# Kernel optimization log

Measured on AMD Instinct MI355X. Metric: run time of the kernel, lower is better.

Reference implementation:

```python
import jax, jax.numpy as jnp
import numpy as np

N = 8192
D_IN = 512
D_OUT = 64
ALPHA = 0.2  # LeakyReLU negative slope
MASK_VAL = -9e15


def setup_inputs() -> dict:
    key = jax.random.key(0)
    k1, k2, k3, k4 = jax.random.split(key, 4)
    inp = jax.random.normal(k1, (N, D_IN), dtype=jnp.float32)
    adj = (jax.random.uniform(k2, (N, N)) < 0.05).astype(jnp.float32)
    adj = adj.at[jnp.arange(N), jnp.arange(N)].set(1.0)
    W = jax.random.normal(k3, (D_IN, D_OUT), dtype=jnp.float32) * 0.05
    a = jax.random.normal(k4, (2 * D_OUT, 1), dtype=jnp.float32) * 0.05
    return {"input": inp, "adj": adj, "W": W, "a": a}


def reference(input, adj, W, a):
    # h = input @ W : [n, out]
    h = input @ W
    # Algebraic equivalent of the dense pairwise concat:
    # e_ij = leakyrelu([h_i || h_j] . a) = leakyrelu(h_i.a1 + h_j.a2)
    a1, a2 = a[:D_OUT, 0], a[D_OUT:, 0]          # [out], [out]
    e = jax.nn.leaky_relu(
        (h @ a1)[:, None] + (h @ a2)[None, :],    # [n, n]
        negative_slope=ALPHA,
    )
    attention = jnp.where(adj > 0, e, MASK_VAL)
    attention = jax.nn.softmax(attention, axis=1)
    out = attention @ h                            # [n, out]
    return jax.nn.elu(out)                         # end=False branch
```

## Files before the change

### kernel.cpp

```cpp
#include <hip/hip_runtime.h>
#include <hip/hip_bf16.h>

#define N 8192
#define D_IN 512
#define D_OUT 64
#define ALPHA 0.2f
#define BM 16
#define NSPLIT 4
#define KSEG (N / NSPLIT)
#define NSH (KSEG / 128)

typedef __attribute__((ext_vector_type(4))) float f32x4;
typedef __attribute__((ext_vector_type(8))) short bf16x8;

static __device__ __forceinline__ unsigned pk_bf16(float lo, float hi) {
    unsigned ulo = __bfloat16_as_ushort(__float2bfloat16(lo));
    unsigned uhi = __bfloat16_as_ushort(__float2bfloat16(hi));
    return (uhi << 16) | ulo;
}

__global__ __launch_bounds__(256) void gat_prep_kernel(
    const float* __restrict__ input, const float* __restrict__ adj,
    const float* __restrict__ W, const float* __restrict__ a,
    unsigned short* __restrict__ hpk, float* __restrict__ s1,
    float* __restrict__ s2, unsigned char* __restrict__ msk)
{
    if (blockIdx.x < 512) {
        int wave = (blockIdx.x * 256 + threadIdx.x) >> 6;
        int lane = threadIdx.x & 63;
        int row0 = wave * 4;
        const float* in0 = input + (size_t)row0 * D_IN;
        float a1 = a[lane], a2 = a[D_OUT + lane];
        float acc[4];
#pragma unroll
        for (int r = 0; r < 4; ++r) acc[r] = 0.f;
#pragma unroll 4
        for (int k = 0; k < D_IN; ++k) {
            float wk = W[k * D_OUT + lane];
#pragma unroll
            for (int r = 0; r < 4; ++r)
                acc[r] = fmaf(in0[(size_t)r * D_IN + k], wk, acc[r]);
        }
        {
            int kw = row0 >> 5, kb = (row0 >> 3) & 3, e0 = row0 & 7;
            int dw = lane >> 4, dd = lane & 15;
            size_t off = ((size_t)((kw * 4 + dw) * 64) + kb * 16 + dd) * 8 + e0;
            uint2 hv;
            hv.x = pk_bf16(acc[0], acc[1]);
            hv.y = pk_bf16(acc[2], acc[3]);
            *(uint2*)(hpk + off) = hv;
        }
#pragma unroll
        for (int r = 0; r < 4; ++r) {
            float p1 = acc[r] * a1;
            float p2 = acc[r] * a2;
#pragma unroll
            for (int off = 32; off; off >>= 1) {
                p1 += __shfl_xor(p1, off, 64);
                p2 += __shfl_xor(p2, off, 64);
            }
            if (lane == 0) { s1[row0 + r] = p1; s2[row0 + r] = p2; }
        }
    } else {
        size_t wave = (((size_t)blockIdx.x - 512) * 256 + threadIdx.x) >> 6;
        int lane = threadIdx.x & 63;
#pragma unroll 4
        for (int it = 0; it < 16; ++it) {
            size_t fo = (wave * 16 + it) * 512 + (size_t)lane * 8;
            float4 v0 = *(const float4*)(adj + fo);
            float4 v1 = *(const float4*)(adj + fo + 4);
            unsigned b =  (unsigned)(v0.x > 0.f)
                       | ((unsigned)(v0.y > 0.f) << 1)
                       | ((unsigned)(v0.z > 0.f) << 2)
                       | ((unsigned)(v0.w > 0.f) << 3)
                       | ((unsigned)(v1.x > 0.f) << 4)
                       | ((unsigned)(v1.y > 0.f) << 5)
                       | ((unsigned)(v1.z > 0.f) << 6)
                       | ((unsigned)(v1.w > 0.f) << 7);
            msk[fo >> 3] = (unsigned char)b;
        }
    }
}

struct MSP { unsigned m; float4 sA, sB; };
struct UBP { uint4 b0, b1, b2, b3; };

static __device__ __forceinline__ void issue_ms(MSP& p, const unsigned char* mb,
                                                const float* sb, int ps) {
    p.m  = mb[ps * 16];
    p.sA = *(const float4*)(sb + ps * 128);
    p.sB = *(const float4*)(sb + ps * 128 + 4);
}
static __device__ __forceinline__ void issue_ub(UBP& p, const unsigned short* hb,
                                                int ps) {
    const unsigned short* f = hb + ((size_t)ps << 13);
    p.b0 = *(const uint4*)(f);
    p.b1 = *(const uint4*)(f + 512);
    p.b2 = *(const uint4*)(f + 1024);
    p.b3 = *(const uint4*)(f + 1536);
}

__global__ __launch_bounds__(256, 4) void gat_flash_kernel(
    const unsigned char* __restrict__ msk, const unsigned short* __restrict__ hpk,
    const float* __restrict__ s1, const float* __restrict__ s2,
    float* __restrict__ pacc, float* __restrict__ plsum)
{
    __shared__ float Cl[4][BM][D_OUT];
    __shared__ float lsl[4][BM];

    const int tid  = threadIdx.x;
    const int lane = tid & 63;
    const int ws   = tid >> 6;
    const int i    = lane & 15;
    const int kb   = lane >> 4;
    const int hf   = blockIdx.x >> 9;
    const int rb   = blockIdx.x & 511;
    const int rg   = rb * BM + i;

    const int col0 = hf * KSEG + ws * 32 + kb * 8;
    const unsigned char* mb_lane = msk + ((size_t)rg << 10) + (col0 >> 3);
    const float* s2_lane = s2 + col0;
    const unsigned short* hb_lane =
        hpk + (((size_t)(hf * 64 + ws)) << 11) + (lane << 3);

    float s1r  = s1[rg];
    float eref = s1r + s2[rg];
    eref = eref > 0.f ? eref : ALPHA * eref;
    float lsum = 0.f;
    f32x4 acc0 = {0,0,0,0}, acc1 = {0,0,0,0}, acc2 = {0,0,0,0}, acc3 = {0,0,0,0};

    auto step = [&](const MSP& p, const UBP& u) {
        const float* sv0 = (const float*)&p.sA;
        const float* sv1 = (const float*)&p.sB;
        float w[8];
#pragma unroll
        for (int z = 0; z < 4; ++z) {
            float e0 = s1r + sv0[z]; e0 = e0 > 0.f ? e0 : ALPHA * e0;
            float e1 = s1r + sv1[z]; e1 = e1 > 0.f ? e1 : ALPHA * e1;
            float w0 = __expf(e0 - eref);
            float w1 = __expf(e1 - eref);
            w[z]     = ((p.m >> z) & 1u)       ? w0 : 0.f;
            w[z + 4] = ((p.m >> (z + 4)) & 1u) ? w1 : 0.f;
        }
#pragma unroll
        for (int z = 0; z < 8; ++z) lsum += w[z];
        uint4 pk;
        pk.x = pk_bf16(w[0], w[1]); pk.y = pk_bf16(w[2], w[3]);
        pk.z = pk_bf16(w[4], w[5]); pk.w = pk_bf16(w[6], w[7]);
        bf16x8 A = __builtin_bit_cast(bf16x8, pk);
        acc0 = __builtin_amdgcn_mfma_f32_16x16x32_bf16(A, __builtin_bit_cast(bf16x8, u.b0), acc0, 0, 0, 0);
        acc1 = __builtin_amdgcn_mfma_f32_16x16x32_bf16(A, __builtin_bit_cast(bf16x8, u.b1), acc1, 0, 0, 0);
        acc2 = __builtin_amdgcn_mfma_f32_16x16x32_bf16(A, __builtin_bit_cast(bf16x8, u.b2), acc2, 0, 0, 0);
        acc3 = __builtin_amdgcn_mfma_f32_16x16x32_bf16(A, __builtin_bit_cast(bf16x8, u.b3), acc3, 0, 0, 0);
    };

    MSP M0, M1; UBP U0, U1;
    issue_ms(M0, mb_lane, s2_lane, 0); issue_ub(U0, hb_lane, 0);
    issue_ms(M1, mb_lane, s2_lane, 1); issue_ub(U1, hb_lane, 1);
#pragma unroll 2
    for (int p = 0; p < NSH; p += 2) {
        step(M0, U0);
        if (p + 2 < NSH) { issue_ms(M0, mb_lane, s2_lane, p + 2); issue_ub(U0, hb_lane, p + 2); }
        step(M1, U1);
        if (p + 3 < NSH) { issue_ms(M1, mb_lane, s2_lane, p + 3); issue_ub(U1, hb_lane, p + 3); }
    }

    lsum += __shfl_xor(lsum, 16, 64);
    lsum += __shfl_xor(lsum, 32, 64);
    if (lane < 16) lsl[ws][lane] = lsum;

    const f32x4 av[4] = {acc0, acc1, acc2, acc3};
#pragma unroll
    for (int dw = 0; dw < 4; ++dw)
#pragma unroll
        for (int reg = 0; reg < 4; ++reg)
            Cl[ws][kb * 4 + reg][dw * 16 + i] = av[dw][reg];
    __syncthreads();

#pragma unroll
    for (int o = tid; o < BM * D_OUT; o += 256) {
        int row = o >> 6, d = o & 63;
        float v = (Cl[0][row][d] + Cl[1][row][d]) + (Cl[2][row][d] + Cl[3][row][d]);
        pacc[((size_t)hf * N + rb * BM + row) * 64 + d] = v;
    }
    if (tid < BM)
        plsum[hf * N + rb * BM + tid] =
            (lsl[0][tid] + lsl[1][tid]) + (lsl[2][tid] + lsl[3][tid]);
}

__global__ __launch_bounds__(256) void gat_reduce_kernel(
    const float* __restrict__ pacc, const float* __restrict__ plsum,
    float* __restrict__ out)
{
    int idx = blockIdx.x * 256 + threadIdx.x;
    int row = idx >> 6;
    float aa = 0.f, l = 0.f;
#pragma unroll
    for (int hf = 0; hf < NSPLIT; ++hf) {
        aa += pacc[(size_t)hf * N * 64 + idx];
        l  += plsum[hf * N + row];
    }
    float o = aa / l;
    out[idx] = o > 0.f ? o : expm1f(o);
}

extern "C" void kernel_launch(void* const* d_in, const int* in_sizes, int n_in,
                              void* d_out, int out_size, void* d_ws, size_t ws_size,
                              hipStream_t stream) {
    const float* input = (const float*)d_in[0];
    const float* adj   = (const float*)d_in[1];
    const float* W     = (const float*)d_in[2];
    const float* a     = (const float*)d_in[3];
    float* out = (float*)d_out;

    unsigned short* hpk = (unsigned short*)d_ws;
    float* s1    = (float*)(hpk + (size_t)N * D_OUT);
    float* s2    = s1 + N;
    float* pacc  = s2 + N;
    float* plsum = pacc + (size_t)NSPLIT * N * 64;
    unsigned char* msk = (unsigned char*)(plsum + NSPLIT * N);

    gat_prep_kernel<<<2560, 256, 0, stream>>>(input, adj, W, a, hpk, s1, s2, msk);
    gat_flash_kernel<<<512 * NSPLIT, 256, 0, stream>>>(msk, hpk, s1, s2, pacc, plsum);
    gat_reduce_kernel<<<N * 64 / 256, 256, 0, stream>>>(pacc, plsum, out);
}
```

Before: 124.1 us.

## Split prep into mask and h kernels, enlarge flash row tile, drop LDS reduction

```diff
diff --git a/kernel.cpp b/kernel.cpp
--- a/kernel.cpp
+++ b/kernel.cpp
@@ -5,10 +5,11 @@
 #define D_IN 512
 #define D_OUT 64
 #define ALPHA 0.2f
-#define BM 16
+#define BM 64
 #define NSPLIT 4
 #define KSEG (N / NSPLIT)
 #define NSH (KSEG / 128)
+#define NSLICE (NSPLIT * 4)
 
 typedef __attribute__((ext_vector_type(4))) float f32x4;
 typedef __attribute__((ext_vector_type(8))) short bf16x8;
@@ -19,75 +20,88 @@
     return (uhi << 16) | ulo;
 }
 
-__global__ __launch_bounds__(256) void gat_prep_kernel(
-    const float* __restrict__ input, const float* __restrict__ adj,
-    const float* __restrict__ W, const float* __restrict__ a,
-    unsigned short* __restrict__ hpk, float* __restrict__ s1,
-    float* __restrict__ s2, unsigned char* __restrict__ msk)
-{
-    if (blockIdx.x < 512) {
-        int wave = (blockIdx.x * 256 + threadIdx.x) >> 6;
-        int lane = threadIdx.x & 63;
-        int row0 = wave * 4;
-        const float* in0 = input + (size_t)row0 * D_IN;
+__global__ __launch_bounds__(256) void gat_mask_kernel(
+    const float* __restrict__ adj, unsigned char* __restrict__ msk)
+{
+    size_t wave = ((size_t)blockIdx.x * 256 + threadIdx.x) >> 6;
+    int lane = threadIdx.x & 63;
+#pragma unroll
+    for (int it = 0; it < 8; ++it) {
+        size_t fo = (wave * 8 + it) * 512 + (size_t)lane * 8;
+        float4 v0 = *(const float4*)(adj + fo);
+        float4 v1 = *(const float4*)(adj + fo + 4);
+        unsigned b =  (unsigned)(v0.x > 0.f)
+                   | ((unsigned)(v0.y > 0.f) << 1)
+                   | ((unsigned)(v0.z > 0.f) << 2)
+                   | ((unsigned)(v0.w > 0.f) << 3)
+                   | ((unsigned)(v1.x > 0.f) << 4)
+                   | ((unsigned)(v1.y > 0.f) << 5)
+                   | ((unsigned)(v1.z > 0.f) << 6)
+                   | ((unsigned)(v1.w > 0.f) << 7);
+        msk[fo >> 3] = (unsigned char)b;
+    }
+}
+
+__global__ __launch_bounds__(256) void gat_h_kernel(
+    const float* __restrict__ input, const float* __restrict__ W,
+    const float* __restrict__ a, unsigned short* __restrict__ hpk,
+    float* __restrict__ s1, float* __restrict__ s2)
+{
+    __shared__ float hp[4][4][64];
+    int ws   = threadIdx.x >> 6;
+    int lane = threadIdx.x & 63;
+    int row0 = blockIdx.x * 4;
+    const float* in0 = input + (size_t)row0 * D_IN + ws * 128;
+    const float* Wp  = W + ws * 128 * D_OUT;
+    float acc[4] = {0.f, 0.f, 0.f, 0.f};
+#pragma unroll 4
+    for (int k = 0; k < 128; ++k) {
+        float wk = Wp[k * D_OUT + lane];
+#pragma unroll
+        for (int r = 0; r < 4; ++r)
+            acc[r] = fmaf(in0[r * D_IN + k], wk, acc[r]);
+    }
+#pragma unroll
+    for (int r = 0; r < 4; ++r) hp[ws][r][lane] = acc[r];
+    __syncthreads();
+    if (ws == 0) {
+        float h[4];
+#pragma unroll
+        for (int r = 0; r < 4; ++r)
+            h[r] = (hp[0][r][lane] + hp[1][r][lane]) + (hp[2][r][lane] + hp[3][r][lane]);
+        int kw = row0 >> 5, kb = (row0 >> 3) & 3, e0 = row0 & 7;
+        int dw = lane >> 4, dd = lane & 15;
+        size_t off = ((size_t)((kw * 4 + dw) * 64) + kb * 16 + dd) * 8 + e0;
+        uint2 hv;
+        hv.x = pk_bf16(h[0], h[1]);
+        hv.y = pk_bf16(h[2], h[3]);
+        *(uint2*)(hpk + off) = hv;
         float a1 = a[lane], a2 = a[D_OUT + lane];
-        float acc[4];
-#pragma unroll
-        for (int r = 0; r < 4; ++r) acc[r] = 0.f;
-#pragma unroll 4
-        for (int k = 0; k < D_IN; ++k) {
-            float wk = W[k * D_OUT + lane];
-#pragma unroll
-            for (int r = 0; r < 4; ++r)
-                acc[r] = fmaf(in0[(size_t)r * D_IN + k], wk, acc[r]);
-        }
-        {
-            int kw = row0 >> 5, kb = (row0 >> 3) & 3, e0 = row0 & 7;
-            int dw = lane >> 4, dd = lane & 15;
-            size_t off = ((size_t)((kw * 4 + dw) * 64) + kb * 16 + dd) * 8 + e0;
-            uint2 hv;
-            hv.x = pk_bf16(acc[0], acc[1]);
-            hv.y = pk_bf16(acc[2], acc[3]);
-            *(uint2*)(hpk + off) = hv;
-        }
 #pragma unroll
         for (int r = 0; r < 4; ++r) {
-            float p1 = acc[r] * a1;
-            float p2 = acc[r] * a2;
-#pragma unroll
-            for (int off = 32; off; off >>= 1) {
-                p1 += __shfl_xor(p1, off, 64);
-                p2 += __shfl_xor(p2, off, 64);
+            float p1 = h[r] * a1;
+            float p2 = h[r] * a2;
+#pragma unroll
+            for (int off2 = 32; off2; off2 >>= 1) {
+                p1 += __shfl_xor(p1, off2, 64);
+                p2 += __shfl_xor(p2, off2, 64);
             }
             if (lane == 0) { s1[row0 + r] = p1; s2[row0 + r] = p2; }
         }
-    } else {
-        size_t wave = (((size_t)blockIdx.x - 512) * 256 + threadIdx.x) >> 6;
-        int lane = threadIdx.x & 63;
-#pragma unroll 4
-        for (int it = 0; it < 16; ++it) {
-            size_t fo = (wave * 16 + it) * 512 + (size_t)lane * 8;
-            float4 v0 = *(const float4*)(adj + fo);
-            float4 v1 = *(const float4*)(adj + fo + 4);
-            unsigned b =  (unsigned)(v0.x > 0.f)
-                       | ((unsigned)(v0.y > 0.f) << 1)
-                       | ((unsigned)(v0.z > 0.f) << 2)
-                       | ((unsigned)(v0.w > 0.f) << 3)
-                       | ((unsigned)(v1.x > 0.f) << 4)
-                       | ((unsigned)(v1.y > 0.f) << 5)
-                       | ((unsigned)(v1.z > 0.f) << 6)
-                       | ((unsigned)(v1.w > 0.f) << 7);
-            msk[fo >> 3] = (unsigned char)b;
-        }
-    }
-}
-
-struct MSP { unsigned m; float4 sA, sB; };
+    }
+}
+
+struct MSP { unsigned m[4]; float4 sA, sB; };
 struct UBP { uint4 b0, b1, b2, b3; };
 
-static __device__ __forceinline__ void issue_ms(MSP& p, const unsigned char* mb,
-                                                const float* sb, int ps) {
-    p.m  = mb[ps * 16];
+static __device__ __forceinline__ void issue_ms(MSP& p,
+    const unsigned char* m0, const unsigned char* m1,
+    const unsigned char* m2, const unsigned char* m3,
+    const float* sb, int ps) {
+    p.m[0] = m0[ps * 16];
+    p.m[1] = m1[ps * 16];
+    p.m[2] = m2[ps * 16];
+    p.m[3] = m3[ps * 16];
     p.sA = *(const float4*)(sb + ps * 128);
     p.sB = *(const float4*)(sb + ps * 128 + 4);
 }
@@ -100,92 +114,103 @@
     p.b3 = *(const uint4*)(f + 1536);
 }
 
-__global__ __launch_bounds__(256, 4) void gat_flash_kernel(
+__global__ __launch_bounds__(256, 2) void gat_flash_kernel(
     const unsigned char* __restrict__ msk, const unsigned short* __restrict__ hpk,
     const float* __restrict__ s1, const float* __restrict__ s2,
     float* __restrict__ pacc, float* __restrict__ plsum)
 {
-    __shared__ float Cl[4][BM][D_OUT];
-    __shared__ float lsl[4][BM];
-
     const int tid  = threadIdx.x;
     const int lane = tid & 63;
     const int ws   = tid >> 6;
     const int i    = lane & 15;
     const int kb   = lane >> 4;
-    const int hf   = blockIdx.x >> 9;
-    const int rb   = blockIdx.x & 511;
-    const int rg   = rb * BM + i;
-
-    const int col0 = hf * KSEG + ws * 32 + kb * 8;
-    const unsigned char* mb_lane = msk + ((size_t)rg << 10) + (col0 >> 3);
-    const float* s2_lane = s2 + col0;
-    const unsigned short* hb_lane =
-        hpk + (((size_t)(hf * 64 + ws)) << 11) + (lane << 3);
-
-    float s1r  = s1[rg];
-    float eref = s1r + s2[rg];
-    eref = eref > 0.f ? eref : ALPHA * eref;
-    float lsum = 0.f;
-    f32x4 acc0 = {0,0,0,0}, acc1 = {0,0,0,0}, acc2 = {0,0,0,0}, acc3 = {0,0,0,0};
+    const int hf   = blockIdx.x >> 7;
+    const int rb   = blockIdx.x & 127;
+    const int r0   = rb * BM;
+
+    const unsigned char* mb0 = msk + ((size_t)(r0 +  0 + i) << 10) + hf * 256 + ws * 4 + kb;
+    const unsigned char* mb1 = msk + ((size_t)(r0 + 16 + i) << 10) + hf * 256 + ws * 4 + kb;
+    const unsigned char* mb2 = msk + ((size_t)(r0 + 32 + i) << 10) + hf * 256 + ws * 4 + kb;
+    const unsigned char* mb3 = msk + ((size_t)(r0 + 48 + i) << 10) + hf * 256 + ws * 4 + kb;
+    const float* s2b = s2 + hf * KSEG + ws * 32 + kb * 8;
+    const unsigned short* hb = hpk + (((size_t)(hf * 64 + ws)) << 11) + (lane << 3);
+
+    float eref[4];
+#pragma unroll
+    for (int ag = 0; ag < 4; ++ag) {
+        int rg = r0 + ag * 16 + i;
+        float e = s1[rg] + s2[rg];
+        eref[ag] = e > 0.f ? e : ALPHA * e;
+    }
+    float s1r[4];
+#pragma unroll
+    for (int ag = 0; ag < 4; ++ag) s1r[ag] = s1[r0 + ag * 16 + i];
+
+    float lsum[4] = {0.f, 0.f, 0.f, 0.f};
+    f32x4 acc[4][4];
+#pragma unroll
+    for (int ag = 0; ag < 4; ++ag)
+#pragma unroll
+        for (int dw = 0; dw < 4; ++dw) acc[ag][dw] = f32x4{0.f, 0.f, 0.f, 0.f};
 
     auto step = [&](const MSP& p, const UBP& u) {
         const float* sv0 = (const float*)&p.sA;
         const float* sv1 = (const float*)&p.sB;
-        float w[8];
-#pragma unroll
-        for (int z = 0; z < 4; ++z) {
-            float e0 = s1r + sv0[z]; e0 = e0 > 0.f ? e0 : ALPHA * e0;
-            float e1 = s1r + sv1[z]; e1 = e1 > 0.f ? e1 : ALPHA * e1;
-            float w0 = __expf(e0 - eref);
-            float w1 = __expf(e1 - eref);
-            w[z]     = ((p.m >> z) & 1u)       ? w0 : 0.f;
-            w[z + 4] = ((p.m >> (z + 4)) & 1u) ? w1 : 0.f;
+        const uint4 ub[4] = {u.b0, u.b1, u.b2, u.b3};
+#pragma unroll
+        for (int ag = 0; ag < 4; ++ag) {
+            float w[8];
+#pragma unroll
+            for (int z = 0; z < 4; ++z) {
+                float e0 = s1r[ag] + sv0[z]; e0 = e0 > 0.f ? e0 : ALPHA * e0;
+                float e1 = s1r[ag] + sv1[z]; e1 = e1 > 0.f ? e1 : ALPHA * e1;
+                float w0 = __expf(e0 - eref[ag]);
+                float w1 = __expf(e1 - eref[ag]);
+                w[z]     = ((p.m[ag] >> z) & 1u)       ? w0 : 0.f;
+                w[z + 4] = ((p.m[ag] >> (z + 4)) & 1u) ? w1 : 0.f;
+            }
+#pragma unroll
+            for (int z = 0; z < 8; ++z) lsum[ag] += w[z];
+            uint4 pk;
+            pk.x = pk_bf16(w[0], w[1]); pk.y = pk_bf16(w[2], w[3]);
+            pk.z = pk_bf16(w[4], w[5]); pk.w = pk_bf16(w[6], w[7]);
+            bf16x8 A = __builtin_bit_cast(bf16x8, pk);
+            acc[ag][0] = __builtin_amdgcn_mfma_f32_16x16x32_bf16(A, __builtin_bit_cast(bf16x8, ub[0]), acc[ag][0], 0, 0, 0);
+            acc[ag][1] = __builtin_amdgcn_mfma_f32_16x16x32_bf16(A, __builtin_bit_cast(bf16x8, ub[1]), acc[ag][1], 0, 0, 0);
+            acc[ag][2] = __builtin_amdgcn_mfma_f32_16x16x32_bf16(A, __builtin_bit_cast(bf16x8, ub[2]), acc[ag][2], 0, 0, 0);
+            acc[ag][3] = __builtin_amdgcn_mfma_f32_16x16x32_bf16(A, __builtin_bit_cast(bf16x8, ub[3]), acc[ag][3], 0, 0, 0);
         }
-#pragma unroll
-        for (int z = 0; z < 8; ++z) lsum += w[z];
-        uint4 pk;
-        pk.x = pk_bf16(w[0], w[1]); pk.y = pk_bf16(w[2], w[3]);
-        pk.z = pk_bf16(w[4], w[5]); pk.w = pk_bf16(w[6], w[7]);
-        bf16x8 A = __builtin_bit_cast(bf16x8, pk);
-        acc0 = __builtin_amdgcn_mfma_f32_16x16x32_bf16(A, __builtin_bit_cast(bf16x8, u.b0), acc0, 0, 0, 0);
-        acc1 = __builtin_amdgcn_mfma_f32_16x16x32_bf16(A, __builtin_bit_cast(bf16x8, u.b1), acc1, 0, 0, 0);
-        acc2 = __builtin_amdgcn_mfma_f32_16x16x32_bf16(A, __builtin_bit_cast(bf16x8, u.b2), acc2, 0, 0, 0);
-        acc3 = __builtin_amdgcn_mfma_f32_16x16x32_bf16(A, __builtin_bit_cast(bf16x8, u.b3), acc3, 0, 0, 0);
     };
 
     MSP M0, M1; UBP U0, U1;
-    issue_ms(M0, mb_lane, s2_lane, 0); issue_ub(U0, hb_lane, 0);
-    issue_ms(M1, mb_lane, s2_lane, 1); issue_ub(U1, hb_lane, 1);
-#pragma unroll 2
+    issue_ms(M0, mb0, mb1, mb2, mb3, s2b, 0); issue_ub(U0, hb, 0);
+    issue_ms(M1, mb0, mb1, mb2, mb3, s2b, 1); issue_ub(U1, hb, 1);
     for (int p = 0; p < NSH; p += 2) {
         step(M0, U0);
-        if (p + 2 < NSH) { issue_ms(M0, mb_lane, s2_lane, p + 2); issue_ub(U0, hb_lane, p + 2); }
+        if (p + 2 < NSH) { issue_ms(M0, mb0, mb1, mb2, mb3, s2b, p + 2); issue_ub(U0, hb, p + 2); }
         step(M1, U1);
-        if (p + 3 < NSH) { issue_ms(M1, mb_lane, s2_lane, p + 3); issue_ub(U1, hb_lane, p + 3); }
-    }
-
-    lsum += __shfl_xor(lsum, 16, 64);
-    lsum += __shfl_xor(lsum, 32, 64);
-    if (lane < 16) lsl[ws][lane] = lsum;
-
-    const f32x4 av[4] = {acc0, acc1, acc2, acc3};
-#pragma unroll
-    for (int dw = 0; dw < 4; ++dw)
-#pragma unroll
-        for (int reg = 0; reg < 4; ++reg)
-            Cl[ws][kb * 4 + reg][dw * 16 + i] = av[dw][reg];
-    __syncthreads();
-
-#pragma unroll
-    for (int o = tid; o < BM * D_OUT; o += 256) {
-        int row = o >> 6, d = o & 63;
-        float v = (Cl[0][row][d] + Cl[1][row][d]) + (Cl[2][row][d] + Cl[3][row][d]);
-        pacc[((size_t)hf * N + rb * BM + row) * 64 + d] = v;
-    }
-    if (tid < BM)
-        plsum[hf * N + rb * BM + tid] =
-            (lsl[0][tid] + lsl[1][tid]) + (lsl[2][tid] + lsl[3][tid]);
+        if (p + 3 < NSH) { issue_ms(M1, mb0, mb1, mb2, mb3, s2b, p + 3); issue_ub(U1, hb, p + 3); }
+    }
+
+#pragma unroll
+    for (int ag = 0; ag < 4; ++ag) {
+        lsum[ag] += __shfl_xor(lsum[ag], 16, 64);
+        lsum[ag] += __shfl_xor(lsum[ag], 32, 64);
+    }
+    const int sp = hf * 4 + ws;
+    if (lane < 16) {
+#pragma unroll
+        for (int ag = 0; ag < 4; ++ag)
+            plsum[(size_t)sp * N + r0 + ag * 16 + lane] = lsum[ag];
+    }
+#pragma unroll
+    for (int ag = 0; ag < 4; ++ag)
+#pragma unroll
+        for (int dw = 0; dw < 4; ++dw)
+#pragma unroll
+            for (int reg = 0; reg < 4; ++reg)
+                pacc[((size_t)sp * N + r0 + ag * 16 + kb * 4 + reg) * 64 + dw * 16 + i]
+                    = acc[ag][dw][reg];
 }
 
 __global__ __launch_bounds__(256) void gat_reduce_kernel(
@@ -196,9 +221,9 @@
     int row = idx >> 6;
     float aa = 0.f, l = 0.f;
 #pragma unroll
-    for (int hf = 0; hf < NSPLIT; ++hf) {
-        aa += pacc[(size_t)hf * N * 64 + idx];
-        l  += plsum[hf * N + row];
+    for (int sp = 0; sp < NSLICE; ++sp) {
+        aa += pacc[(size_t)sp * N * 64 + idx];
+        l  += plsum[(size_t)sp * N + row];
     }
     float o = aa / l;
     out[idx] = o > 0.f ? o : expm1f(o);
@@ -217,10 +242,11 @@
     float* s1    = (float*)(hpk + (size_t)N * D_OUT);
     float* s2    = s1 + N;
     float* pacc  = s2 + N;
-    float* plsum = pacc + (size_t)NSPLIT * N * 64;
-    unsigned char* msk = (unsigned char*)(plsum + NSPLIT * N);
-
-    gat_prep_kernel<<<2560, 256, 0, stream>>>(input, adj, W, a, hpk, s1, s2, msk);
-    gat_flash_kernel<<<512 * NSPLIT, 256, 0, stream>>>(msk, hpk, s1, s2, pacc, plsum);
+    float* plsum = pacc + (size_t)NSLICE * N * 64;
+    unsigned char* msk = (unsigned char*)(plsum + (size_t)NSLICE * N);
+
+    gat_mask_kernel<<<4096, 256, 0, stream>>>(adj, msk);
+    gat_h_kernel<<<2048, 256, 0, stream>>>(input, W, a, hpk, s1, s2);
+    gat_flash_kernel<<<128 * NSPLIT, 256, 0, stream>>>(msk, hpk, s1, s2, pacc, plsum);
     gat_reduce_kernel<<<N * 64 / 256, 256, 0, stream>>>(pacc, plsum, out);
 }
```

Result: slower. 139.9 us (+12.8%).
